# Performance work log

Hardware: AMD Instinct MI355X
Metric: run time of the kernel (lower is better)

The kernel has to match this reference:

```python
import jax, jax.numpy as jnp
import numpy as np

N_HEADS = 16
DIM = 1024
HW = 32
B = 8


def _conv3x3(x, W, b):
    # x: [B, C, H, W], W: [O, I, 3, 3] (OIHW), padding 1 == SAME for stride 1
    y = jax.lax.conv_general_dilated(
        x, W, window_strides=(1, 1), padding='SAME',
        dimension_numbers=('NCHW', 'OIHW', 'NCHW'))
    return y + b[None, :, None, None]


def setup_inputs() -> dict:
    key = jax.random.key(0)
    ks = jax.random.split(key, 8)
    f32 = jnp.float32
    q = jax.random.normal(ks[0], (B, DIM, HW, HW), f32)
    k = jax.random.normal(ks[1], (B, DIM, HW, HW), f32)
    v = jax.random.normal(ks[2], (B, DIM, HW, HW), f32)
    Wq = jax.random.normal(ks[3], (DIM, DIM, 3, 3), f32) * 0.02
    Wk = jax.random.normal(ks[4], (DIM, DIM, 3, 3), f32) * 0.02
    Wv = jax.random.normal(ks[5], (DIM, DIM, 3, 3), f32) * 0.02
    Wo = jax.random.normal(ks[6], (DIM, DIM), f32) * 0.02
    bq = jnp.zeros((DIM,), f32); bk = jnp.zeros((DIM,), f32)
    bv = jnp.zeros((DIM,), f32); bo = jnp.zeros((DIM,), f32)
    mask = jax.random.randint(ks[7], (B, DIM, DIM), 0, 2, jnp.int32)
    return {'q': q, 'k': k, 'v': v, 'Wq': Wq, 'bq': bq, 'Wk': Wk, 'bk': bk,
            'Wv': Wv, 'bv': bv, 'Wo': Wo, 'bo': bo, 'mask': mask}


def reference(q, k, v, Wq, bq, Wk, bk, Wv, bv, Wo, bo, mask):
    Bq, C, H, W = q.shape  # C == dim, tokens = channels
    h = N_HEADS
    d = (H * W) // h  # head dim

    def split_heads(x):
        # [B, C, H, W] -> [B, h, C, d]
        return x.reshape(Bq, C, h, d).transpose(0, 2, 1, 3)

    qh = split_heads(_conv3x3(q, Wq, bq))
    kh = split_heads(_conv3x3(k, Wk, bk))
    vh = split_heads(_conv3x3(v, Wv, bv))

    scale = 1.0 / np.sqrt(d).astype(np.float32)
    attn = jnp.einsum('bhtd,bhsd->bhts', qh, kh) * scale  # [B, h, C, C]
    attn = jnp.where(mask[:, None, :, :] == 0, jnp.float32(-1e9), attn)
    w = jax.nn.softmax(attn, axis=-1)  # attn_dropout rate = 0 -> identity
    out = jnp.einsum('bhts,bhsd->bhtd', w, vh)  # [B, h, C, d]
    out = out.transpose(0, 2, 1, 3).reshape(Bq, C, h * d)  # [B, C, H*W]
    out = out @ Wo.T + bo  # Linear(dim, dim); H*W == dim
    return out
```

## Files before the change

kernel.cpp:

```cpp
#include <hip/hip_runtime.h>

typedef __attribute__((ext_vector_type(8))) short bh8;
typedef __attribute__((ext_vector_type(4))) short bh4;
typedef __attribute__((ext_vector_type(4))) float f32x4;

__device__ __forceinline__ short f2bf(float f) {
  union { float f; unsigned u; } a; a.f = f;
  unsigned r = a.u + 0x7FFFu + ((a.u >> 16) & 1u);
  return (short)(r >> 16);
}

__device__ __forceinline__ void g2l16(const short* g, short* l) {
  __builtin_amdgcn_global_load_lds(
      (const __attribute__((address_space(1))) void*)g,
      (__attribute__((address_space(3))) void*)l, 16, 0, 0);
}

__global__ __launch_bounds__(256) void zero16(short* p, int n8) {
  int i = blockIdx.x * 256 + threadIdx.x;
  if (i < n8) { bh8 z = {0, 0, 0, 0, 0, 0, 0, 0}; ((bh8*)p)[i] = z; }
}

__global__ __launch_bounds__(256) void transpose3(
    const float* __restrict__ q, const float* __restrict__ k, const float* __restrict__ v,
    short* __restrict__ qP, short* __restrict__ kP, short* __restrict__ vP) {
  int z = blockIdx.z; int tensor = z >> 3, b = z & 7;
  const float* src = tensor == 0 ? q : (tensor == 1 ? k : v);
  short* dst = tensor == 0 ? qP : (tensor == 1 ? kP : vP);
  src += (size_t)b * 1048576; dst += (size_t)b * 1183744;
  int row0 = blockIdx.y * 64;
  int col0 = blockIdx.x * 64;
  __shared__ short t[64][72];
  int tid = threadIdx.x;
#pragma unroll
  for (int i = 0; i < 2; ++i) {
    int cid = tid + i * 256;
    int r = cid >> 3, co = (cid & 7) * 8;
    const float* p = src + (size_t)(row0 + r) * 1024 + col0 + co;
    float4 f0 = *(const float4*)(p);
    float4 f1 = *(const float4*)(p + 4);
    t[co + 0][r] = f2bf(f0.x); t[co + 1][r] = f2bf(f0.y);
    t[co + 2][r] = f2bf(f0.z); t[co + 3][r] = f2bf(f0.w);
    t[co + 4][r] = f2bf(f1.x); t[co + 5][r] = f2bf(f1.y);
    t[co + 6][r] = f2bf(f1.z); t[co + 7][r] = f2bf(f1.w);
  }
  __syncthreads();
#pragma unroll
  for (int i = 0; i < 2; ++i) {
    int cid = tid + i * 256;
    int sr = cid >> 3, cc = (cid & 7) * 8;
    bh8 val = *(const bh8*)&t[sr][cc];
    int tok = col0 + sr;
    int pr = ((tok >> 5) + 1) * 34 + (tok & 31) + 1;
    *(bh8*)(dst + (size_t)pr * 1024 + row0 + cc) = val;
  }
}

__global__ __launch_bounds__(256) void wperm3(
    const float* __restrict__ Wq, const float* __restrict__ Wk, const float* __restrict__ Wv,
    short* __restrict__ WpQ, short* __restrict__ WpK, short* __restrict__ WpV) {
  int z = blockIdx.y;
  const float* W = z == 0 ? Wq : (z == 1 ? Wk : Wv);
  short* Wp = z == 0 ? WpQ : (z == 1 ? WpK : WpV);
  int idx = blockIdx.x * 256 + threadIdx.x;
  const float* wsrc = W + (size_t)idx * 9;
#pragma unroll
  for (int t = 0; t < 9; ++t) Wp[(size_t)t * 1048576 + idx] = f2bf(wsrc[t]);
}

__global__ __launch_bounds__(256) void cvt_bf(const float* __restrict__ src,
                                              short* __restrict__ dst) {
  int idx = (blockIdx.x * 256 + threadIdx.x) * 4;
  float4 f = *(const float4*)(src + idx);
  bh4 o; o[0] = f2bf(f.x); o[1] = f2bf(f.y); o[2] = f2bf(f.z); o[3] = f2bf(f.w);
  *(bh4*)(dst + idx) = o;
}

__global__ __launch_bounds__(256) void mask_pack(const int* __restrict__ m,
                                                 unsigned* __restrict__ mp) {
  int idx = blockIdx.x * 256 + threadIdx.x;
  const int* src = m + (size_t)idx * 32;
  unsigned wv = 0;
#pragma unroll
  for (int j = 0; j < 32; j += 4) {
    int4 a = *(const int4*)(src + j);
    wv |= ((unsigned)(a.x & 1) << j) | ((unsigned)(a.y & 1) << (j + 1)) |
          ((unsigned)(a.z & 1) << (j + 2)) | ((unsigned)(a.w & 1) << (j + 3));
  }
  mp[idx] = wv;
}

__global__ __launch_bounds__(256) void conv_gemm_all(
    const short* __restrict__ WpQ, const short* __restrict__ WpK, const short* __restrict__ WpV,
    const short* __restrict__ xPq, const short* __restrict__ xPk, const short* __restrict__ xPv,
    short* __restrict__ cQ, short* __restrict__ cK, short* __restrict__ cVT,
    const float* __restrict__ bq, const float* __restrict__ bk, const float* __restrict__ bv,
    int convSel) {
  __shared__ short sA[4096];
  __shared__ short sB[4096];
  int tid = threadIdx.x, lane = tid & 63, w = tid >> 6;
  int z = blockIdx.z;
  int conv = convSel >= 0 ? convSel : (z >> 3);
  int b = convSel >= 0 ? z : (z & 7);
  const short* Wp = conv == 0 ? WpQ : (conv == 1 ? WpK : WpV);
  const short* xP = conv == 0 ? xPq : (conv == 1 ? xPk : xPv);
  short* out = conv == 0 ? cQ : (conv == 1 ? cK : cVT);
  const float* bias = conv == 0 ? bq : (conv == 1 ? bk : bv);
  int XisA = (conv == 2);
  int mbase = blockIdx.x * 128, nbase = blockIdx.y * 128;
  const short* xb = xP + (size_t)b * 1183744;
  int wbase = XisA ? nbase : mbase;
  int sbase = XisA ? mbase : nbase;
  short* sW = XisA ? sB : sA;
  short* sX = XisA ? sA : sB;

  int colsh = (lane & 3) * 8;
  int ldsoff[2]; const short* wp0[2]; const short* xp0[2];
#pragma unroll
  for (int i = 0; i < 2; ++i) {
    int row = 32 * w + 16 * i + (lane >> 2);
    ldsoff[i] = (2 * w + i) * 512 + lane * 8;
    wp0[i] = Wp + (size_t)(wbase + row) * 1024 + colsh;
    int tok = sbase + row;
    int pr0 = ((tok >> 5) + 1) * 34 + (tok & 31) + 1;
    xp0[i] = xb + (size_t)pr0 * 1024 + colsh;
  }
  f32x4 acc[4][4] = {};
  int wm = (w >> 1) * 64, wn = (w & 1) * 64;
  for (int tap = 0; tap < 9; ++tap) {
    int dOff = (tap / 3 - 1) * 34 + (tap % 3 - 1);
    size_t wtap = (size_t)tap * 1048576;
    for (int kt = 0; kt < 1024; kt += 32) {
#pragma unroll
      for (int i = 0; i < 2; ++i) {
        g2l16(wp0[i] + wtap + kt, sW + ldsoff[i]);
        g2l16(xp0[i] + (ptrdiff_t)dOff * 1024 + kt, sX + ldsoff[i]);
      }
      __syncthreads();
      bh8 af[4], bfr[4];
#pragma unroll
      for (int mt = 0; mt < 4; ++mt)
        af[mt] = *(const bh8*)&sA[(wm + mt * 16 + (lane & 15)) * 32 + (lane >> 4) * 8];
#pragma unroll
      for (int nt = 0; nt < 4; ++nt)
        bfr[nt] = *(const bh8*)&sB[(wn + nt * 16 + (lane & 15)) * 32 + (lane >> 4) * 8];
#pragma unroll
      for (int mt = 0; mt < 4; ++mt)
#pragma unroll
        for (int nt = 0; nt < 4; ++nt)
          acc[mt][nt] = __builtin_amdgcn_mfma_f32_16x16x32_bf16(af[mt], bfr[nt], acc[mt][nt], 0, 0, 0);
      __syncthreads();
    }
  }
  size_t ob = (size_t)b * 1048576;
#pragma unroll
  for (int mt = 0; mt < 4; ++mt) {
#pragma unroll
    for (int nt = 0; nt < 4; ++nt) {
      int m0 = mbase + wm + mt * 16 + ((lane >> 4) << 2);
      int n = nbase + wn + nt * 16 + (lane & 15);
#pragma unroll
      for (int r = 0; r < 4; ++r) {
        float bv = bias[XisA ? n : (m0 + r)];
        out[ob + (size_t)(m0 + r) * 1024 + n] = f2bf(acc[mt][nt][r] + bv);
      }
    }
  }
}

__global__ __launch_bounds__(256) void attn(
    const short* __restrict__ Qc, const short* __restrict__ Kc,
    const short* __restrict__ VT, const unsigned* __restrict__ Mp,
    short* __restrict__ AO) {
  __shared__ short sQ[64][72];
  __shared__ short sK[128][72];
  __shared__ short sV[64][136];
  __shared__ short sP[64][136];
  int tid = threadIdx.x, lane = tid & 63, w = tid >> 6;
  int qbase = blockIdx.x * 64, h = blockIdx.y, b = blockIdx.z;
  int j0 = h * 64;
  const short* Qb = Qc + (size_t)b * 1048576;
  const short* Kb = Kc + (size_t)b * 1048576;
  const short* Vb = VT + (size_t)b * 1048576;
  const unsigned* Mpb = Mp + (size_t)b * 32768;
  const float scale = 0.125f;

#pragma unroll
  for (int i = 0; i < 2; ++i) {
    int cid = tid + i * 256;
    int row = cid >> 3, co = (cid & 7) * 8;
    *(bh8*)&sQ[row][co] = *(const bh8*)(Qb + (size_t)(qbase + row) * 1024 + j0 + co);
  }
  __syncthreads();

  int tg = qbase + w * 16 + (lane & 15);
  float mrow = -3.0e38f, lrow = 0.0f;

  for (int st = 0; st < 8; ++st) {
#pragma unroll
    for (int i = 0; i < 4; ++i) {
      int cid = tid + i * 256;
      int row = cid >> 3, co = (cid & 7) * 8;
      *(bh8*)&sK[row][co] = *(const bh8*)(Kb + (size_t)(st * 128 + row) * 1024 + j0 + co);
    }
    __syncthreads();
    f32x4 sacc[8];
#pragma unroll
    for (int mt = 0; mt < 8; ++mt) {
      f32x4 a = {0.f, 0.f, 0.f, 0.f};
      bh8 kf = *(const bh8*)&sK[mt * 16 + (lane & 15)][(lane >> 4) * 8];
      bh8 qf = *(const bh8*)&sQ[w * 16 + (lane & 15)][(lane >> 4) * 8];
      a = __builtin_amdgcn_mfma_f32_16x16x32_bf16(kf, qf, a, 0, 0, 0);
      kf = *(const bh8*)&sK[mt * 16 + (lane & 15)][32 + (lane >> 4) * 8];
      qf = *(const bh8*)&sQ[w * 16 + (lane & 15)][32 + (lane >> 4) * 8];
      a = __builtin_amdgcn_mfma_f32_16x16x32_bf16(kf, qf, a, 0, 0, 0);
      sacc[mt] = a;
    }
    float tmax = -3.0e38f;
#pragma unroll
    for (int mt = 0; mt < 8; ++mt) {
      int sb = st * 128 + mt * 16 + ((lane >> 4) << 2);
      unsigned mw = Mpb[(size_t)tg * 32 + (sb >> 5)] >> (sb & 31);
      f32x4 vv;
      vv[0] = (mw & 1u) ? sacc[mt][0] * scale : -1e9f;
      vv[1] = (mw & 2u) ? sacc[mt][1] * scale : -1e9f;
      vv[2] = (mw & 4u) ? sacc[mt][2] * scale : -1e9f;
      vv[3] = (mw & 8u) ? sacc[mt][3] * scale : -1e9f;
      sacc[mt] = vv;
      tmax = fmaxf(tmax, fmaxf(fmaxf(vv[0], vv[1]), fmaxf(vv[2], vv[3])));
    }
    tmax = fmaxf(tmax, __shfl_xor(tmax, 16, 64));
    tmax = fmaxf(tmax, __shfl_xor(tmax, 32, 64));
    float mnew = fmaxf(mrow, tmax);
    float sum = 0.f;
#pragma unroll
    for (int mt = 0; mt < 8; ++mt)
#pragma unroll
      for (int r = 0; r < 4; ++r) sum += __expf(fminf(sacc[mt][r] - mnew, 0.f));
    sum += __shfl_xor(sum, 16, 64);
    sum += __shfl_xor(sum, 32, 64);
    lrow = lrow * __expf(fminf(mrow - mnew, 0.f)) + sum;
    mrow = mnew;
    __syncthreads();
  }
  float rl = 1.0f / lrow;

  f32x4 oacc[4] = {};
  for (int st = 0; st < 8; ++st) {
#pragma unroll
    for (int i = 0; i < 4; ++i) {
      int cid = tid + i * 256;
      int row = cid >> 3, co = (cid & 7) * 8;
      *(bh8*)&sK[row][co] = *(const bh8*)(Kb + (size_t)(st * 128 + row) * 1024 + j0 + co);
      int vrow = cid >> 4, vco = (cid & 15) * 8;
      *(bh8*)&sV[vrow][vco] = *(const bh8*)(Vb + (size_t)(j0 + vrow) * 1024 + st * 128 + vco);
    }
    __syncthreads();
#pragma unroll
    for (int mt = 0; mt < 8; ++mt) {
      f32x4 a = {0.f, 0.f, 0.f, 0.f};
      bh8 kf = *(const bh8*)&sK[mt * 16 + (lane & 15)][(lane >> 4) * 8];
      bh8 qf = *(const bh8*)&sQ[w * 16 + (lane & 15)][(lane >> 4) * 8];
      a = __builtin_amdgcn_mfma_f32_16x16x32_bf16(kf, qf, a, 0, 0, 0);
      kf = *(const bh8*)&sK[mt * 16 + (lane & 15)][32 + (lane >> 4) * 8];
      qf = *(const bh8*)&sQ[w * 16 + (lane & 15)][32 + (lane >> 4) * 8];
      a = __builtin_amdgcn_mfma_f32_16x16x32_bf16(kf, qf, a, 0, 0, 0);
      int sb = mt * 16 + ((lane >> 4) << 2);
      unsigned mw = Mpb[(size_t)tg * 32 + ((st * 128 + sb) >> 5)] >> (sb & 31);
      bh4 p;
      p[0] = (mw & 1u) ? f2bf(__expf(fminf(a[0] * scale - mrow, 0.f)) * rl) : (short)0;
      p[1] = (mw & 2u) ? f2bf(__expf(fminf(a[1] * scale - mrow, 0.f)) * rl) : (short)0;
      p[2] = (mw & 4u) ? f2bf(__expf(fminf(a[2] * scale - mrow, 0.f)) * rl) : (short)0;
      p[3] = (mw & 8u) ? f2bf(__expf(fminf(a[3] * scale - mrow, 0.f)) * rl) : (short)0;
      *(bh4*)&sP[w * 16 + (lane & 15)][sb] = p;
    }
    __syncthreads();
#pragma unroll
    for (int k0 = 0; k0 < 4; ++k0) {
      bh8 pf = *(const bh8*)&sP[w * 16 + (lane & 15)][k0 * 32 + (lane >> 4) * 8];
#pragma unroll
      for (int nt = 0; nt < 4; ++nt) {
        bh8 vf = *(const bh8*)&sV[nt * 16 + (lane & 15)][k0 * 32 + (lane >> 4) * 8];
        oacc[nt] = __builtin_amdgcn_mfma_f32_16x16x32_bf16(pf, vf, oacc[nt], 0, 0, 0);
      }
    }
    __syncthreads();
  }
  size_t ob = (size_t)b * 1048576;
#pragma unroll
  for (int nt = 0; nt < 4; ++nt) {
    int j = nt * 16 + (lane & 15);
    int t0 = qbase + w * 16 + ((lane >> 4) << 2);
#pragma unroll
    for (int r = 0; r < 4; ++r)
      AO[ob + (size_t)(t0 + r) * 1024 + j0 + j] = f2bf(oacc[nt][r]);
  }
}

__global__ __launch_bounds__(256) void gemm_bt(
    const short* __restrict__ A, const short* __restrict__ Bm,
    float* __restrict__ out, const float* __restrict__ bias) {
  __shared__ short sA[4096];
  __shared__ short sB[4096];
  int tid = threadIdx.x, lane = tid & 63, w = tid >> 6;
  int mbase = blockIdx.x * 128, nbase = blockIdx.y * 128;
  int colsh = (lane & 3) * 8;
  int ldsoff[2]; const short* ap[2]; const short* bp[2];
#pragma unroll
  for (int i = 0; i < 2; ++i) {
    int row = 32 * w + 16 * i + (lane >> 2);
    ldsoff[i] = (2 * w + i) * 512 + lane * 8;
    ap[i] = A + (size_t)(mbase + row) * 1024 + colsh;
    bp[i] = Bm + (size_t)(nbase + row) * 1024 + colsh;
  }
  f32x4 acc[4][4] = {};
  int wm = (w >> 1) * 64, wn = (w & 1) * 64;
  for (int kt = 0; kt < 1024; kt += 32) {
#pragma unroll
    for (int i = 0; i < 2; ++i) {
      g2l16(ap[i] + kt, sA + ldsoff[i]);
      g2l16(bp[i] + kt, sB + ldsoff[i]);
    }
    __syncthreads();
    bh8 af[4], bfr[4];
#pragma unroll
    for (int mt = 0; mt < 4; ++mt)
      af[mt] = *(const bh8*)&sA[(wm + mt * 16 + (lane & 15)) * 32 + (lane >> 4) * 8];
#pragma unroll
    for (int nt = 0; nt < 4; ++nt)
      bfr[nt] = *(const bh8*)&sB[(wn + nt * 16 + (lane & 15)) * 32 + (lane >> 4) * 8];
#pragma unroll
    for (int mt = 0; mt < 4; ++mt)
#pragma unroll
      for (int nt = 0; nt < 4; ++nt)
        acc[mt][nt] = __builtin_amdgcn_mfma_f32_16x16x32_bf16(af[mt], bfr[nt], acc[mt][nt], 0, 0, 0);
    __syncthreads();
  }
#pragma unroll
  for (int mt = 0; mt < 4; ++mt) {
#pragma unroll
    for (int nt = 0; nt < 4; ++nt) {
      int m0 = mbase + wm + mt * 16 + ((lane >> 4) << 2);
      int n = nbase + wn + nt * 16 + (lane & 15);
      float bv = bias[n];
#pragma unroll
      for (int r = 0; r < 4; ++r)
        out[(size_t)(m0 + r) * 1024 + n] = acc[mt][nt][r] + bv;
    }
  }
}

extern "C" void kernel_launch(void* const* d_in, const int* in_sizes, int n_in,
                              void* d_out, int out_size, void* d_ws, size_t ws_size,
                              hipStream_t stream) {
  (void)in_sizes; (void)n_in; (void)out_size;
  const float* q    = (const float*)d_in[0];
  const float* k    = (const float*)d_in[1];
  const float* v    = (const float*)d_in[2];
  const float* Wq   = (const float*)d_in[3];
  const float* bq   = (const float*)d_in[4];
  const float* Wk   = (const float*)d_in[5];
  const float* bk   = (const float*)d_in[6];
  const float* Wv   = (const float*)d_in[7];
  const float* bv   = (const float*)d_in[8];
  const float* Wo   = (const float*)d_in[9];
  const float* bo   = (const float*)d_in[10];
  const int*   mask = (const int*)d_in[11];
  float* out = (float*)d_out;
  char* ws = (char*)d_ws;

  const size_t XPE = 1156ull * 1024 * 8;
  const size_t XPB = XPE * 2;
  const size_t WPE = 9ull * 1048576;
  short* xPq = (short*)ws;
  short* xPk = xPq + XPE;
  short* xPv = xPk + XPE;
  short* WpQ = (short*)(ws + 3 * XPB);
  short* WpK = WpQ + WPE;
  short* WpV = WpK + WPE;
  char* p2 = ws + 3 * XPB + 3 * WPE * 2;

  bool fused = ws_size >= 167000000ull;
  short *cQ, *cK, *cVT, *WoB, *AO; unsigned* Mpk;
  if (fused) {
    cQ  = (short*)(p2);
    cK  = (short*)(p2 + 16777216);
    cVT = (short*)(p2 + 33554432);
    WoB = (short*)(p2 + 50331648);
    Mpk = (unsigned*)(p2 + 52428800);
    AO  = xPq;
  } else {
    cQ  = (short*)(p2);
    WoB = (short*)(p2 + 16777216);
    Mpk = (unsigned*)(p2 + 18874368);
    cK  = xPq;
    cVT = xPk;
    AO  = xPv;
  }

  zero16<<<dim3(13872), dim3(256), 0, stream>>>(xPq, 3551232);
  transpose3<<<dim3(16, 16, 24), dim3(256), 0, stream>>>(q, k, v, xPq, xPk, xPv);
  wperm3<<<dim3(4096, 3), dim3(256), 0, stream>>>(Wq, Wk, Wv, WpQ, WpK, WpV);
  cvt_bf<<<dim3(1024), dim3(256), 0, stream>>>(Wo, WoB);
  mask_pack<<<dim3(1024), dim3(256), 0, stream>>>(mask, Mpk);
  if (fused) {
    conv_gemm_all<<<dim3(8, 8, 24), dim3(256), 0, stream>>>(
        WpQ, WpK, WpV, xPq, xPk, xPv, cQ, cK, cVT, bq, bk, bv, -1);
  } else {
    conv_gemm_all<<<dim3(8, 8, 8), dim3(256), 0, stream>>>(
        WpQ, WpK, WpV, xPq, xPk, xPv, cQ, cK, cVT, bq, bk, bv, 0);
    conv_gemm_all<<<dim3(8, 8, 8), dim3(256), 0, stream>>>(
        WpQ, WpK, WpV, xPq, xPk, xPv, cQ, cK, cVT, bq, bk, bv, 1);
    conv_gemm_all<<<dim3(8, 8, 8), dim3(256), 0, stream>>>(
        WpQ, WpK, WpV, xPq, xPk, xPv, cQ, cK, cVT, bq, bk, bv, 2);
  }
  attn<<<dim3(16, 16, 8), dim3(256), 0, stream>>>(cQ, cK, cVT, Mpk, AO);
  gemm_bt<<<dim3(64, 8), dim3(256), 0, stream>>>(AO, WoB, out, bo);
}
```

Measured before the change: 974.6 us.

## Use single-pass online softmax in attention and zero only conv halo

Measured after the change: 925.6 us. 1.05x faster.

```diff
diff --git a/kernel.cpp b/kernel.cpp
--- a/kernel.cpp
+++ b/kernel.cpp
@@ -16,9 +16,17 @@
       (__attribute__((address_space(3))) void*)l, 16, 0, 0);
 }
 
-__global__ __launch_bounds__(256) void zero16(short* p, int n8) {
-  int i = blockIdx.x * 256 + threadIdx.x;
-  if (i < n8) { bh8 z = {0, 0, 0, 0, 0, 0, 0, 0}; ((bh8*)p)[i] = z; }
+__global__ __launch_bounds__(256) void zero_halo(short* __restrict__ xP) {
+  int z = blockIdx.y;
+  short* base = xP + (size_t)z * 1183744;
+  int ri = blockIdx.x * 2 + (threadIdx.x >> 7);
+  int row;
+  if (ri < 34) row = ri;
+  else if (ri < 68) row = 1122 + (ri - 34);
+  else { int j = ri - 68; int y = (j >> 1) + 1; int x = (j & 1) ? 33 : 0; row = y * 34 + x; }
+  int col = (threadIdx.x & 127) * 8;
+  bh8 zv = {0, 0, 0, 0, 0, 0, 0, 0};
+  *(bh8*)(base + (size_t)row * 1024 + col) = zv;
 }
 
 __global__ __launch_bounds__(256) void transpose3(
@@ -194,7 +202,9 @@
   __syncthreads();
 
   int tg = qbase + w * 16 + (lane & 15);
+  int rsel = ((lane >> 4) << 2);
   float mrow = -3.0e38f, lrow = 0.0f;
+  f32x4 oacc[4] = {};
 
   for (int st = 0; st < 8; ++st) {
 #pragma unroll
@@ -202,8 +212,11 @@
       int cid = tid + i * 256;
       int row = cid >> 3, co = (cid & 7) * 8;
       *(bh8*)&sK[row][co] = *(const bh8*)(Kb + (size_t)(st * 128 + row) * 1024 + j0 + co);
+      int vrow = cid >> 4, vco = (cid & 15) * 8;
+      *(bh8*)&sV[vrow][vco] = *(const bh8*)(Vb + (size_t)(j0 + vrow) * 1024 + st * 128 + vco);
     }
     __syncthreads();
+
     f32x4 sacc[8];
 #pragma unroll
     for (int mt = 0; mt < 8; ++mt) {
@@ -216,65 +229,52 @@
       a = __builtin_amdgcn_mfma_f32_16x16x32_bf16(kf, qf, a, 0, 0, 0);
       sacc[mt] = a;
     }
+
+    uint4 Mw = *(const uint4*)(Mpb + (size_t)tg * 32 + st * 4);
     float tmax = -3.0e38f;
 #pragma unroll
     for (int mt = 0; mt < 8; ++mt) {
-      int sb = st * 128 + mt * 16 + ((lane >> 4) << 2);
-      unsigned mw = Mpb[(size_t)tg * 32 + (sb >> 5)] >> (sb & 31);
+      unsigned mwv = ((const unsigned*)&Mw)[mt >> 1] >> ((mt & 1) * 16 + rsel);
       f32x4 vv;
-      vv[0] = (mw & 1u) ? sacc[mt][0] * scale : -1e9f;
-      vv[1] = (mw & 2u) ? sacc[mt][1] * scale : -1e9f;
-      vv[2] = (mw & 4u) ? sacc[mt][2] * scale : -1e9f;
-      vv[3] = (mw & 8u) ? sacc[mt][3] * scale : -1e9f;
+      vv[0] = (mwv & 1u) ? sacc[mt][0] * scale : -1e9f;
+      vv[1] = (mwv & 2u) ? sacc[mt][1] * scale : -1e9f;
+      vv[2] = (mwv & 4u) ? sacc[mt][2] * scale : -1e9f;
+      vv[3] = (mwv & 8u) ? sacc[mt][3] * scale : -1e9f;
       sacc[mt] = vv;
       tmax = fmaxf(tmax, fmaxf(fmaxf(vv[0], vv[1]), fmaxf(vv[2], vv[3])));
     }
     tmax = fmaxf(tmax, __shfl_xor(tmax, 16, 64));
     tmax = fmaxf(tmax, __shfl_xor(tmax, 32, 64));
     float mnew = fmaxf(mrow, tmax);
+    float alpha = __expf(fminf(mrow - mnew, 0.f));
+
     float sum = 0.f;
-#pragma unroll
-    for (int mt = 0; mt < 8; ++mt)
-#pragma unroll
-      for (int r = 0; r < 4; ++r) sum += __expf(fminf(sacc[mt][r] - mnew, 0.f));
+    uint4 Mw2 = Mw;
+#pragma unroll
+    for (int mt = 0; mt < 8; ++mt) {
+      unsigned mwv = ((const unsigned*)&Mw2)[mt >> 1] >> ((mt & 1) * 16 + rsel);
+      float p0 = (mwv & 1u) ? __expf(fminf(sacc[mt][0] - mnew, 0.f)) : 0.f;
+      float p1 = (mwv & 2u) ? __expf(fminf(sacc[mt][1] - mnew, 0.f)) : 0.f;
+      float p2 = (mwv & 4u) ? __expf(fminf(sacc[mt][2] - mnew, 0.f)) : 0.f;
+      float p3 = (mwv & 8u) ? __expf(fminf(sacc[mt][3] - mnew, 0.f)) : 0.f;
+      sum += (p0 + p1) + (p2 + p3);
+      bh4 p; p[0] = f2bf(p0); p[1] = f2bf(p1); p[2] = f2bf(p2); p[3] = f2bf(p3);
+      *(bh4*)&sP[w * 16 + (lane & 15)][mt * 16 + rsel] = p;
+    }
     sum += __shfl_xor(sum, 16, 64);
     sum += __shfl_xor(sum, 32, 64);
-    lrow = lrow * __expf(fminf(mrow - mnew, 0.f)) + sum;
+    lrow = lrow * alpha + sum;
     mrow = mnew;
+
+    float al[4];
+#pragma unroll
+    for (int r = 0; r < 4; ++r) al[r] = __shfl(alpha, rsel + r, 64);
+#pragma unroll
+    for (int nt = 0; nt < 4; ++nt)
+#pragma unroll
+      for (int r = 0; r < 4; ++r) oacc[nt][r] *= al[r];
     __syncthreads();
-  }
-  float rl = 1.0f / lrow;
-
-  f32x4 oacc[4] = {};
-  for (int st = 0; st < 8; ++st) {
-#pragma unroll
-    for (int i = 0; i < 4; ++i) {
-      int cid = tid + i * 256;
-      int row = cid >> 3, co = (cid & 7) * 8;
-      *(bh8*)&sK[row][co] = *(const bh8*)(Kb + (size_t)(st * 128 + row) * 1024 + j0 + co);
-      int vrow = cid >> 4, vco = (cid & 15) * 8;
-      *(bh8*)&sV[vrow][vco] = *(const bh8*)(Vb + (size_t)(j0 + vrow) * 1024 + st * 128 + vco);
-    }
-    __syncthreads();
-#pragma unroll
-    for (int mt = 0; mt < 8; ++mt) {
-      f32x4 a = {0.f, 0.f, 0.f, 0.f};
-      bh8 kf = *(const bh8*)&sK[mt * 16 + (lane & 15)][(lane >> 4) * 8];
-      bh8 qf = *(const bh8*)&sQ[w * 16 + (lane & 15)][(lane >> 4) * 8];
-      a = __builtin_amdgcn_mfma_f32_16x16x32_bf16(kf, qf, a, 0, 0, 0);
-      kf = *(const bh8*)&sK[mt * 16 + (lane & 15)][32 + (lane >> 4) * 8];
-      qf = *(const bh8*)&sQ[w * 16 + (lane & 15)][32 + (lane >> 4) * 8];
-      a = __builtin_amdgcn_mfma_f32_16x16x32_bf16(kf, qf, a, 0, 0, 0);
-      int sb = mt * 16 + ((lane >> 4) << 2);
-      unsigned mw = Mpb[(size_t)tg * 32 + ((st * 128 + sb) >> 5)] >> (sb & 31);
-      bh4 p;
-      p[0] = (mw & 1u) ? f2bf(__expf(fminf(a[0] * scale - mrow, 0.f)) * rl) : (short)0;
-      p[1] = (mw & 2u) ? f2bf(__expf(fminf(a[1] * scale - mrow, 0.f)) * rl) : (short)0;
-      p[2] = (mw & 4u) ? f2bf(__expf(fminf(a[2] * scale - mrow, 0.f)) * rl) : (short)0;
-      p[3] = (mw & 8u) ? f2bf(__expf(fminf(a[3] * scale - mrow, 0.f)) * rl) : (short)0;
-      *(bh4*)&sP[w * 16 + (lane & 15)][sb] = p;
-    }
-    __syncthreads();
+
 #pragma unroll
     for (int k0 = 0; k0 < 4; ++k0) {
       bh8 pf = *(const bh8*)&sP[w * 16 + (lane & 15)][k0 * 32 + (lane >> 4) * 8];
@@ -286,14 +286,18 @@
     }
     __syncthreads();
   }
+
+  float rl[4];
+#pragma unroll
+  for (int r = 0; r < 4; ++r) rl[r] = 1.0f / __shfl(lrow, rsel + r, 64);
   size_t ob = (size_t)b * 1048576;
 #pragma unroll
   for (int nt = 0; nt < 4; ++nt) {
     int j = nt * 16 + (lane & 15);
-    int t0 = qbase + w * 16 + ((lane >> 4) << 2);
+    int t0 = qbase + w * 16 + rsel;
 #pragma unroll
     for (int r = 0; r < 4; ++r)
-      AO[ob + (size_t)(t0 + r) * 1024 + j0 + j] = f2bf(oacc[nt][r]);
+      AO[ob + (size_t)(t0 + r) * 1024 + j0 + j] = f2bf(oacc[nt][r] * rl[r]);
   }
 }
 
@@ -398,7 +402,7 @@
     AO  = xPv;
   }
 
-  zero16<<<dim3(13872), dim3(256), 0, stream>>>(xPq, 3551232);
+  zero_halo<<<dim3(66, 24), dim3(256), 0, stream>>>(xPq);
   transpose3<<<dim3(16, 16, 24), dim3(256), 0, stream>>>(q, k, v, xPq, xPk, xPv);
   wperm3<<<dim3(4096, 3), dim3(256), 0, stream>>>(Wq, Wk, Wv, WpQ, WpK, WpV);
   cvt_bf<<<dim3(1024), dim3(256), 0, stream>>>(Wo, WoB);
```
